# Optimization experiments

Hardware: AMD Instinct MI355X
Metric: run time of the kernel (lower is better)

The kernel has to match this reference:

```python
import jax, jax.numpy as jnp
import numpy as np

H = 16  # num_heads
LN_EPS = 1e-5


def setup_inputs() -> dict:
    key = jax.random.key(0)
    ks = jax.random.split(key, 9)
    B, Lq, Lkv, D = 8, 512, 1024, 1024
    s = 1.0 / np.sqrt(D)
    return {
        "query": jax.random.normal(ks[0], (B, Lq, D), dtype=jnp.float32),
        "key": jax.random.normal(ks[1], (B, Lkv, D), dtype=jnp.float32),
        "value": jax.random.normal(ks[2], (B, Lkv, D), dtype=jnp.float32),
        "in_proj_w": jax.random.normal(ks[3], (3 * D, D), dtype=jnp.float32) * s,
        "in_proj_b": jnp.zeros((3 * D,), dtype=jnp.float32),
        "out_proj_w": jax.random.normal(ks[4], (D, D), dtype=jnp.float32) * s,
        "out_proj_b": jnp.zeros((D,), dtype=jnp.float32),
        "ln_gamma": jnp.ones((D,), dtype=jnp.float32),
        "ln_beta": jnp.zeros((D,), dtype=jnp.float32),
    }


def reference(query, key, value, in_proj_w, in_proj_b, out_proj_w, out_proj_b, ln_gamma, ln_beta):
    B, Lq, D = query.shape
    Lkv = key.shape[1]
    hd = D // H
    wq, wk, wv = jnp.split(in_proj_w, 3, axis=0)   # each [D, D]
    bq, bk, bv = jnp.split(in_proj_b, 3, axis=0)

    def heads(x, L):
        return x.reshape(B, L, H, hd).transpose(0, 2, 1, 3)  # [B,H,L,hd]

    q = heads(query @ wq.T + bq, Lq) * (1.0 / np.sqrt(hd))
    k = heads(key @ wk.T + bk, Lkv)
    v = heads(value @ wv.T + bv, Lkv)

    scores = jnp.einsum('bhqd,bhkd->bhqk', q, k)           # [B,H,Lq,Lkv]
    attn = jax.nn.softmax(scores, axis=-1)
    # attention dropout: identity in eval mode
    ctx = jnp.einsum('bhqk,bhkd->bhqd', attn, v)           # [B,H,Lq,hd]
    ctx = ctx.transpose(0, 2, 1, 3).reshape(B, Lq, D)
    attn_out = ctx @ out_proj_w.T + out_proj_b

    # residual dropout: identity in eval mode; then LayerNorm
    x = query + attn_out
    mu = jnp.mean(x, axis=-1, keepdims=True)
    var = jnp.mean(jnp.square(x - mu), axis=-1, keepdims=True)
    output = (x - mu) * jax.lax.rsqrt(var + LN_EPS) * ln_gamma + ln_beta

    attn_weights = attn.mean(axis=1)                        # avg over heads [B,Lq,Lkv]
    return (output, attn_weights)
```

## Files before the change

kernel.cpp:

```cpp
#include <hip/hip_runtime.h>
#include <stdint.h>

typedef __attribute__((ext_vector_type(8))) short short8;
typedef __attribute__((ext_vector_type(4))) float f32x4;

#define DEV static __device__ __forceinline__

DEV unsigned short f2bf(float f) {
    union { float f; unsigned int u; } v; v.f = f;
    unsigned int u = v.u;
    return (unsigned short)((u + 0x7fffu + ((u >> 16) & 1u)) >> 16);
}

DEV float bf2f(unsigned short s) {
    union { unsigned int u; float f; } v; v.u = ((unsigned int)s) << 16;
    return v.f;
}

DEV void async_lds16(const void* g, void* l) {
    __builtin_amdgcn_global_load_lds(
        (const __attribute__((address_space(1))) unsigned int*)g,
        (__attribute__((address_space(3))) unsigned int*)l, 16, 0, 0);
}

__global__ __launch_bounds__(256)
void k_cvt_all(const float* __restrict__ s0, unsigned short* __restrict__ d0,
               const float* __restrict__ s1, unsigned short* __restrict__ d1,
               const float* __restrict__ s2, unsigned short* __restrict__ d2,
               const float* __restrict__ s3, unsigned short* __restrict__ d3,
               const float* __restrict__ s4, unsigned short* __restrict__ d4)
{
    const float* srcs[5] = {s0, s1, s2, s3, s4};
    unsigned short* dsts[5] = {d0, d1, d2, d3, d4};
    const int n4s[5] = {4096 * 256, 8192 * 256, 8192 * 256, 3072 * 256, 1024 * 256};
    int tid = blockIdx.x * 256 + threadIdx.x;
    int stride = gridDim.x * 256;
#pragma unroll
    for (int seg = 0; seg < 5; ++seg) {
        const float* in = srcs[seg];
        unsigned short* out = dsts[seg];
        int n4 = n4s[seg];
        for (int i = tid; i < n4; i += stride) {
            float4 v = ((const float4*)in)[i];
            ushort4 o;
            o.x = f2bf(v.x); o.y = f2bf(v.y); o.z = f2bf(v.z); o.w = f2bf(v.w);
            ((ushort4*)out)[i] = o;
        }
    }
}

template<typename EpiF>
DEV void gemm_core(const unsigned short* __restrict__ A,
                   const unsigned short* __restrict__ Bm,
                   const float* __restrict__ bias,
                   int row0, int col0,
                   unsigned short* As, unsigned short* Bs,
                   EpiF epi)
{
    const int t = threadIdx.x;
    const int lane = t & 63, w = t >> 6;
    const int i16 = lane & 15, g = lane >> 4;
    const int wr = w >> 1, wc = w & 1;
    const int K = 1024;

    f32x4 acc[4][4];
#pragma unroll
    for (int a = 0; a < 4; ++a)
#pragma unroll
        for (int b = 0; b < 4; ++b) acc[a][b] = f32x4{0.f, 0.f, 0.f, 0.f};

    for (int kt = 0; kt < K / 64; ++kt) {
        const unsigned short* Ag = A + (size_t)row0 * K + kt * 64;
        const unsigned short* Bg = Bm + (size_t)col0 * K + kt * 64;
#pragma unroll
        for (int s = 0; s < 4; ++s) {
            int ch = s * 256 + t;
            int r = ch >> 3, cb = (ch & 7) * 8;
            async_lds16(Ag + (size_t)r * K + cb, &As[ch * 8]);
            async_lds16(Bg + (size_t)r * K + cb, &Bs[ch * 8]);
        }
        __syncthreads();
#pragma unroll
        for (int ks = 0; ks < 2; ++ks) {
            short8 af[4], bfr[4];
#pragma unroll
            for (int mi = 0; mi < 4; ++mi)
                af[mi] = *(const short8*)&As[(wr * 64 + mi * 16 + i16) * 64 + ks * 32 + g * 8];
#pragma unroll
            for (int ni = 0; ni < 4; ++ni)
                bfr[ni] = *(const short8*)&Bs[(wc * 64 + ni * 16 + i16) * 64 + ks * 32 + g * 8];
#pragma unroll
            for (int mi = 0; mi < 4; ++mi)
#pragma unroll
                for (int ni = 0; ni < 4; ++ni)
                    acc[mi][ni] = __builtin_amdgcn_mfma_f32_16x16x32_bf16(af[mi], bfr[ni], acc[mi][ni], 0, 0, 0);
        }
        __syncthreads();
    }

#pragma unroll
    for (int mi = 0; mi < 4; ++mi)
#pragma unroll
        for (int ni = 0; ni < 4; ++ni)
#pragma unroll
            for (int r = 0; r < 4; ++r) {
                int row = row0 + wr * 64 + mi * 16 + g * 4 + r;
                int col = col0 + wc * 64 + ni * 16 + i16;
                epi(row, col, acc[mi][ni][r] + bias[col]);
            }
}

__global__ __launch_bounds__(256)
void k_gemm_qkv(const unsigned short* __restrict__ Aq,
                const unsigned short* __restrict__ Ak,
                const unsigned short* __restrict__ Av,
                const unsigned short* __restrict__ Bm,
                const float* __restrict__ inb,
                unsigned short* __restrict__ q_flat,
                unsigned short* __restrict__ k_heads,
                unsigned short* __restrict__ vt_heads)
{
    __shared__ unsigned short As[128 * 64];
    __shared__ unsigned short Bs[128 * 64];
    const int z = blockIdx.z;
    if (z == 0 && blockIdx.x >= 32) return;
    const int row0 = blockIdx.x * 128;
    const int col0 = blockIdx.y * 128;
    const unsigned short* A = (z == 0) ? Aq : (z == 1) ? Ak : Av;
    const unsigned short* B = Bm + (size_t)z * 1024 * 1024;
    const float* bias = inb + z * 1024;

    if (z == 0) {
        gemm_core(A, B, bias, row0, col0, As, Bs,
            [&](int row, int col, float v) {
                q_flat[(size_t)row * 1024 + col] = f2bf(v * 0.125f);
            });
    } else if (z == 1) {
        gemm_core(A, B, bias, row0, col0, As, Bs,
            [&](int row, int col, float v) {
                int bb = row >> 10, kv = row & 1023, h = col >> 6, d = col & 63;
                size_t addr = (size_t)(bb * 16 + h) * 65536
                            + (size_t)(kv >> 4) * 1024 + (d >> 5) * 512
                            + ((d >> 3) & 3) * 128 + (kv & 15) * 8 + (d & 7);
                k_heads[addr] = f2bf(v);
            });
    } else {
        gemm_core(A, B, bias, row0, col0, As, Bs,
            [&](int row, int col, float v) {
                int bb = row >> 10, kv = row & 1023, h = col >> 6, d = col & 63;
                size_t addr = (size_t)(bb * 16 + h) * 65536
                            + (size_t)(kv >> 5) * 2048 + ((kv >> 3) & 3) * 512
                            + (d >> 4) * 128 + (d & 15) * 8 + (kv & 7);
                vt_heads[addr] = f2bf(v);
            });
    }
}

__global__ __launch_bounds__(256)
void k_gemm_out(const unsigned short* __restrict__ A,
                const unsigned short* __restrict__ Bm,
                const float* __restrict__ bias,
                const float* __restrict__ resid,
                float* __restrict__ Cout)
{
    __shared__ unsigned short As[128 * 64];
    __shared__ unsigned short Bs[128 * 64];
    const int row0 = blockIdx.x * 128;
    const int col0 = blockIdx.y * 128;
    gemm_core(A, Bm, bias, row0, col0, As, Bs,
        [&](int row, int col, float v) {
            Cout[(size_t)row * 1024 + col] = v + resid[(size_t)row * 1024 + col];
        });
}

__global__ __launch_bounds__(512)
void k_attn(const unsigned short* __restrict__ qf,
            const unsigned short* __restrict__ kh,
            const unsigned short* __restrict__ vt,
            unsigned short* __restrict__ ctx,
            unsigned short* __restrict__ attw_part)
{
    __shared__ unsigned short q_lds[16 * 256];
    __shared__ unsigned short p_lds[16 * 1024];
    __shared__ float ctxbuf[16][68];
    __shared__ float redsum[8][16];
    __shared__ float gsum[16];

    const int t = threadIdx.x;
    const int lane = t & 63, w = t >> 6;
    const int i16 = lane & 15, g = lane >> 4;
    const int bid = blockIdx.x;
    const int logical = (bid & 7) * 128 + (bid >> 3);
    const int qt = logical & 31;
    const int bh = logical >> 5;
    const int b = bh >> 2, hg = bh & 3;
    const int q0 = qt * 16;
    const int wn = w & 3, khf = w >> 2;

    {
        const unsigned short* qg = qf + ((size_t)(b * 512 + q0)) * 1024 + hg * 256;
        int q = t >> 5, c = t & 31;
        int sc = (c * 8) ^ ((q & 7) << 3);
        async_lds16(qg + (size_t)q * 1024 + sc, &q_lds[t * 8]);
    }
    __syncthreads();

    float attw_acc[8][4];
#pragma unroll
    for (int mt = 0; mt < 8; ++mt)
#pragma unroll
        for (int r = 0; r < 4; ++r) attw_acc[mt][r] = 0.f;

    for (int hh = 0; hh < 4; ++hh) {
        const int h = hg * 4 + hh;
        short8 qb0, qb1;
        {
            int sw = (i16 & 7) << 4;
            const char* qb = (const char*)q_lds + i16 * 512;
            qb0 = *(const short8*)(qb + ((hh * 128 + g * 16) ^ sw));
            qb1 = *(const short8*)(qb + ((hh * 128 + 64 + g * 16) ^ sw));
        }
        const unsigned short* kbase = kh + (size_t)(b * 16 + h) * 65536
                                    + (size_t)w * 8192 + g * 128 + i16 * 8;
        f32x4 c[8];
#pragma unroll
        for (int mt = 0; mt < 8; ++mt) c[mt] = f32x4{0.f, 0.f, 0.f, 0.f};
#pragma unroll
        for (int mt = 0; mt < 8; ++mt) {
            short8 a0 = *(const short8*)(kbase + mt * 1024);
            short8 a1 = *(const short8*)(kbase + mt * 1024 + 512);
            c[mt] = __builtin_amdgcn_mfma_f32_16x16x32_bf16(a0, qb0, c[mt], 0, 0, 0);
            c[mt] = __builtin_amdgcn_mfma_f32_16x16x32_bf16(a1, qb1, c[mt], 0, 0, 0);
        }
        float s = 0.f;
#pragma unroll
        for (int mt = 0; mt < 8; ++mt)
#pragma unroll
            for (int r = 0; r < 4; ++r) {
                float ev = __expf(c[mt][r]);
                c[mt][r] = ev;
                s += ev;
            }
        s += __shfl_xor(s, 16);
        s += __shfl_xor(s, 32);
        if (lane < 16) redsum[w][lane] = s;
#pragma unroll
        for (int mt = 0; mt < 8; ++mt) {
            unsigned int lo = (unsigned int)f2bf(c[mt][0]) | ((unsigned int)f2bf(c[mt][1]) << 16);
            unsigned int hi = (unsigned int)f2bf(c[mt][2]) | ((unsigned int)f2bf(c[mt][3]) << 16);
            uint2 pk; pk.x = lo; pk.y = hi;
            int pwb = (i16 * 2048 + w * 256 + mt * 32 + g * 8) ^ ((i16 & 7) << 4);
            *(uint2*)((char*)p_lds + pwb) = pk;
        }
        __syncthreads();
        float gs = 0.f;
#pragma unroll
        for (int ww = 0; ww < 8; ++ww) gs += redsum[ww][i16];
        if (w == 0 && lane < 16) gsum[lane] = gs;
        float rs16 = 0.0625f / gs;
#pragma unroll
        for (int mt = 0; mt < 8; ++mt)
#pragma unroll
            for (int r = 0; r < 4; ++r) attw_acc[mt][r] += c[mt][r] * rs16;
        const unsigned short* vbase = vt + (size_t)(b * 16 + h) * 65536
                                    + (size_t)khf * 32768 + g * 512 + wn * 128 + i16 * 8;
        f32x4 cc0 = f32x4{0.f, 0.f, 0.f, 0.f};
        f32x4 cc1 = f32x4{0.f, 0.f, 0.f, 0.f};
#pragma unroll
        for (int kt = 0; kt < 16; kt += 2) {
            short8 pa0 = *(const short8*)((const char*)p_lds
                          + ((i16 * 2048 + khf * 1024 + kt * 64 + g * 16) ^ ((i16 & 7) << 4)));
            short8 vv0 = *(const short8*)(vbase + kt * 2048);
            cc0 = __builtin_amdgcn_mfma_f32_16x16x32_bf16(pa0, vv0, cc0, 0, 0, 0);
            short8 pa1 = *(const short8*)((const char*)p_lds
                          + ((i16 * 2048 + khf * 1024 + (kt + 1) * 64 + g * 16) ^ ((i16 & 7) << 4)));
            short8 vv1 = *(const short8*)(vbase + (kt + 1) * 2048);
            cc1 = __builtin_amdgcn_mfma_f32_16x16x32_bf16(pa1, vv1, cc1, 0, 0, 0);
        }
        if (khf == 0) {
#pragma unroll
            for (int r = 0; r < 4; ++r) ctxbuf[g * 4 + r][wn * 16 + i16] = cc0[r] + cc1[r];
        }
        __syncthreads();
        if (khf == 1) {
#pragma unroll
            for (int r = 0; r < 4; ++r) {
                int q = g * 4 + r;
                float v = cc0[r] + cc1[r] + ctxbuf[q][wn * 16 + i16];
                ctx[((size_t)b * 512 + q0 + q) * 1024 + h * 64 + wn * 16 + i16] = f2bf(v / gsum[q]);
            }
        }
    }

    unsigned short* pw = attw_part + (size_t)hg * (8u * 512u * 1024u)
                       + ((size_t)(b * 512 + q0 + i16)) * 1024;
#pragma unroll
    for (int mt = 0; mt < 8; ++mt) {
        ushort4 o;
        o.x = f2bf(attw_acc[mt][0]); o.y = f2bf(attw_acc[mt][1]);
        o.z = f2bf(attw_acc[mt][2]); o.w = f2bf(attw_acc[mt][3]);
        int kv = w * 128 + mt * 16 + g * 4;
        *(ushort4*)&pw[kv] = o;
    }
}

__global__ __launch_bounds__(256)
void k_attw_red(const unsigned short* __restrict__ part, float* __restrict__ attw) {
    const size_t GSTRIDE = (size_t)8 * 512 * 1024;
    int n4 = (int)(GSTRIDE / 4);
    int i = blockIdx.x * 256 + threadIdx.x;
    int stride = gridDim.x * 256;
    for (; i < n4; i += stride) {
        float4 acc = {0.f, 0.f, 0.f, 0.f};
#pragma unroll
        for (int gp = 0; gp < 4; ++gp) {
            ushort4 u = ((const ushort4*)(part + gp * GSTRIDE))[i];
            acc.x += bf2f(u.x); acc.y += bf2f(u.y);
            acc.z += bf2f(u.z); acc.w += bf2f(u.w);
        }
        ((float4*)attw)[i] = acc;
    }
}

__global__ __launch_bounds__(256)
void k_ln(const float* __restrict__ x, const float* __restrict__ gamma,
          const float* __restrict__ beta, float* __restrict__ out)
{
    int row = blockIdx.x;
    const float* xr = x + (size_t)row * 1024;
    int t = threadIdx.x;
    float4 v = ((const float4*)xr)[t];
    float s = v.x + v.y + v.z + v.w;
    float sq = v.x * v.x + v.y * v.y + v.z * v.z + v.w * v.w;
#pragma unroll
    for (int o = 32; o > 0; o >>= 1) { s += __shfl_xor(s, o); sq += __shfl_xor(sq, o); }
    __shared__ float rs[4], rq[4];
    int w = t >> 6;
    if ((t & 63) == 0) { rs[w] = s; rq[w] = sq; }
    __syncthreads();
    s = rs[0] + rs[1] + rs[2] + rs[3];
    sq = rq[0] + rq[1] + rq[2] + rq[3];
    float mu = s * (1.f / 1024.f);
    float var = sq * (1.f / 1024.f) - mu * mu;
    float rstd = rsqrtf(var + 1e-5f);
    float4 gm = ((const float4*)gamma)[t];
    float4 bt = ((const float4*)beta)[t];
    float4 o;
    o.x = (v.x - mu) * rstd * gm.x + bt.x;
    o.y = (v.y - mu) * rstd * gm.y + bt.y;
    o.z = (v.z - mu) * rstd * gm.z + bt.z;
    o.w = (v.w - mu) * rstd * gm.w + bt.w;
    ((float4*)(out + (size_t)row * 1024))[t] = o;
}

extern "C" void kernel_launch(void* const* d_in, const int* in_sizes, int n_in,
                              void* d_out, int out_size, void* d_ws, size_t ws_size,
                              hipStream_t stream) {
    const float* query = (const float*)d_in[0];
    const float* key   = (const float*)d_in[1];
    const float* value = (const float*)d_in[2];
    const float* inw   = (const float*)d_in[3];
    const float* inb   = (const float*)d_in[4];
    const float* outw  = (const float*)d_in[5];
    const float* outb  = (const float*)d_in[6];
    const float* lng   = (const float*)d_in[7];
    const float* lnb   = (const float*)d_in[8];

    char* ws = (char*)d_ws;
    unsigned short* query_bf = (unsigned short*)(ws);
    unsigned short* key_bf   = (unsigned short*)(ws + ((size_t)8 << 20));
    unsigned short* value_bf = (unsigned short*)(ws + ((size_t)24 << 20));
    unsigned short* inw_bf   = (unsigned short*)(ws + ((size_t)40 << 20));
    unsigned short* outw_bf  = (unsigned short*)(ws + ((size_t)46 << 20));
    unsigned short* q_flat   = (unsigned short*)(ws + ((size_t)48 << 20));
    unsigned short* k_heads  = (unsigned short*)(ws + ((size_t)56 << 20));
    unsigned short* vt_heads = (unsigned short*)(ws + ((size_t)72 << 20));
    unsigned short* ctx_bf   = query_bf;
    unsigned short* attw_part= key_bf;
    float*          x_f32    = (float*)(ws + ((size_t)24 << 20));

    float* out0 = (float*)d_out;
    float* attw = out0 + (size_t)4096 * 1024;

    k_cvt_all<<<dim3(2048), dim3(256), 0, stream>>>(
        query, query_bf, key, key_bf, value, value_bf, inw, inw_bf, outw, outw_bf);

    k_gemm_qkv<<<dim3(64, 8, 3), dim3(256), 0, stream>>>(
        query_bf, key_bf, value_bf, inw_bf, inb, q_flat, k_heads, vt_heads);

    k_attn<<<dim3(1024), dim3(512), 0, stream>>>(q_flat, k_heads, vt_heads, ctx_bf, attw_part);
    k_attw_red<<<dim3(2048), dim3(256), 0, stream>>>(attw_part, attw);

    k_gemm_out<<<dim3(32, 8), dim3(256), 0, stream>>>(ctx_bf, outw_bf, outb, query, x_f32);
    k_ln<<<dim3(4096), dim3(256), 0, stream>>>(x_f32, lng, lnb, out0);
}
```

Baseline: 341.3 us.

## Stage K/V GEMM epilogues through LDS, remap grid, shrink out-proj tiles

The QKV GEMM epilogue for K and V now writes the bf16 results into LDS in the head-blocked layout, then copies them to global memory as contiguous 16-byte stores, replacing scattered 2-byte writes. The grid becomes 1D with a blockIdx remap that drops the idle z==0 blocks and interleaves tiles across XCDs. The output projection moves to 128x64 tiles with 512 blocks to raise occupancy on the small 4096x1024 GEMM. The cost is an extra LDS round trip and barrier in the epilogue.

```diff
diff --git a/kernel.cpp b/kernel.cpp
--- a/kernel.cpp
+++ b/kernel.cpp
@@ -49,13 +49,12 @@
     }
 }
 
-template<typename EpiF>
+template<typename FinF>
 DEV void gemm_core(const unsigned short* __restrict__ A,
                    const unsigned short* __restrict__ Bm,
-                   const float* __restrict__ bias,
                    int row0, int col0,
                    unsigned short* As, unsigned short* Bs,
-                   EpiF epi)
+                   FinF finish)
 {
     const int t = threadIdx.x;
     const int lane = t & 63, w = t >> 6;
@@ -97,17 +96,7 @@
         }
         __syncthreads();
     }
-
-#pragma unroll
-    for (int mi = 0; mi < 4; ++mi)
-#pragma unroll
-        for (int ni = 0; ni < 4; ++ni)
-#pragma unroll
-            for (int r = 0; r < 4; ++r) {
-                int row = row0 + wr * 64 + mi * 16 + g * 4 + r;
-                int col = col0 + wc * 64 + ni * 16 + i16;
-                epi(row, col, acc[mi][ni][r] + bias[col]);
-            }
+    finish(acc);
 }
 
 __global__ __launch_bounds__(256)
@@ -120,38 +109,97 @@
                 unsigned short* __restrict__ k_heads,
                 unsigned short* __restrict__ vt_heads)
 {
-    __shared__ unsigned short As[128 * 64];
-    __shared__ unsigned short Bs[128 * 64];
-    const int z = blockIdx.z;
-    if (z == 0 && blockIdx.x >= 32) return;
-    const int row0 = blockIdx.x * 128;
-    const int col0 = blockIdx.y * 128;
+    __shared__ __align__(16) unsigned short As[128 * 64];
+    __shared__ __align__(16) unsigned short Bs[128 * 64];
+    const int t = threadIdx.x;
+    const int lane = t & 63, w = t >> 6;
+    const int i16 = lane & 15, g = lane >> 4;
+    const int wr = w >> 1, wc = w & 1;
+
+    int l = (blockIdx.x & 7) * 160 + (blockIdx.x >> 3);
+    int z, x, y;
+    if (l < 256)      { z = 0; x = l & 31; y = l >> 5; }
+    else if (l < 768) { z = 1; l -= 256; x = l & 63; y = l >> 6; }
+    else              { z = 2; l -= 768; x = l & 63; y = l >> 6; }
+    const int row0 = x * 128;
+    const int col0 = y * 128;
     const unsigned short* A = (z == 0) ? Aq : (z == 1) ? Ak : Av;
     const unsigned short* B = Bm + (size_t)z * 1024 * 1024;
     const float* bias = inb + z * 1024;
 
     if (z == 0) {
-        gemm_core(A, B, bias, row0, col0, As, Bs,
-            [&](int row, int col, float v) {
-                q_flat[(size_t)row * 1024 + col] = f2bf(v * 0.125f);
+        gemm_core(A, B, row0, col0, As, Bs,
+            [&](const f32x4 (&acc)[4][4]) {
+#pragma unroll
+                for (int mi = 0; mi < 4; ++mi)
+#pragma unroll
+                    for (int ni = 0; ni < 4; ++ni)
+#pragma unroll
+                        for (int r = 0; r < 4; ++r) {
+                            int row = row0 + wr * 64 + mi * 16 + g * 4 + r;
+                            int col = col0 + wc * 64 + ni * 16 + i16;
+                            q_flat[(size_t)row * 1024 + col] = f2bf((acc[mi][ni][r] + bias[col]) * 0.125f);
+                        }
             });
     } else if (z == 1) {
-        gemm_core(A, B, bias, row0, col0, As, Bs,
-            [&](int row, int col, float v) {
-                int bb = row >> 10, kv = row & 1023, h = col >> 6, d = col & 63;
-                size_t addr = (size_t)(bb * 16 + h) * 65536
-                            + (size_t)(kv >> 4) * 1024 + (d >> 5) * 512
-                            + ((d >> 3) & 3) * 128 + (kv & 15) * 8 + (d & 7);
-                k_heads[addr] = f2bf(v);
+        gemm_core(A, B, row0, col0, As, Bs,
+            [&](const f32x4 (&acc)[4][4]) {
+                unsigned short* stg = wc ? Bs : As;
+#pragma unroll
+                for (int mi = 0; mi < 4; ++mi)
+#pragma unroll
+                    for (int ni = 0; ni < 4; ++ni)
+#pragma unroll
+                        for (int r = 0; r < 4; ++r) {
+                            int lkv = wr * 64 + mi * 16 + g * 4 + r;
+                            int d = ni * 16 + i16;
+                            float v = acc[mi][ni][r] + bias[col0 + wc * 64 + d];
+                            int loc = (lkv >> 4) * 1024 + (d >> 5) * 512
+                                    + ((d >> 3) & 3) * 128 + (lkv & 15) * 8 + (d & 7);
+                            stg[loc] = f2bf(v);
+                        }
+                __syncthreads();
+                int bb = row0 >> 10, h0 = col0 >> 6;
+                size_t base = (size_t)(bb * 16 + h0) * 65536 + (size_t)((row0 & 1023) >> 4) * 1024;
+                short8* d0 = (short8*)(k_heads + base);
+                short8* d1 = (short8*)(k_heads + base + 65536);
+#pragma unroll
+                for (int i = 0; i < 4; ++i) {
+                    d0[i * 256 + t] = ((const short8*)As)[i * 256 + t];
+                    d1[i * 256 + t] = ((const short8*)Bs)[i * 256 + t];
+                }
             });
     } else {
-        gemm_core(A, B, bias, row0, col0, As, Bs,
-            [&](int row, int col, float v) {
-                int bb = row >> 10, kv = row & 1023, h = col >> 6, d = col & 63;
-                size_t addr = (size_t)(bb * 16 + h) * 65536
-                            + (size_t)(kv >> 5) * 2048 + ((kv >> 3) & 3) * 512
-                            + (d >> 4) * 128 + (d & 15) * 8 + (kv & 7);
-                vt_heads[addr] = f2bf(v);
+        gemm_core(A, B, row0, col0, As, Bs,
+            [&](const f32x4 (&acc)[4][4]) {
+                unsigned short* stg = wc ? Bs : As;
+#pragma unroll
+                for (int mi = 0; mi < 4; ++mi)
+#pragma unroll
+                    for (int ni = 0; ni < 4; ++ni) {
+                        int lkv0 = wr * 64 + mi * 16 + g * 4;
+                        int d = ni * 16 + i16;
+                        float v0 = acc[mi][ni][0] + bias[col0 + wc * 64 + d];
+                        float v1 = acc[mi][ni][1] + bias[col0 + wc * 64 + d];
+                        float v2 = acc[mi][ni][2] + bias[col0 + wc * 64 + d];
+                        float v3 = acc[mi][ni][3] + bias[col0 + wc * 64 + d];
+                        int loc = (lkv0 >> 5) * 2048 + ((lkv0 >> 3) & 3) * 512
+                                + (d >> 4) * 128 + (d & 15) * 8 + (lkv0 & 7);
+                        uint2 pk;
+                        pk.x = (unsigned int)f2bf(v0) | ((unsigned int)f2bf(v1) << 16);
+                        pk.y = (unsigned int)f2bf(v2) | ((unsigned int)f2bf(v3) << 16);
+                        *(uint2*)&stg[loc] = pk;
+                    }
+                __syncthreads();
+                int bb = row0 >> 10, h0 = col0 >> 6;
+                size_t base = (size_t)(bb * 16 + h0) * 65536 + (size_t)((row0 & 1023) >> 5) * 2048;
+                short8* d0 = (short8*)(vt_heads + base);
+                short8* d1 = (short8*)(vt_heads + base + 65536);
+#pragma unroll
+                for (int i = 0; i < 4; ++i) {
+                    d0[i * 256 + t] = ((const short8*)As)[i * 256 + t];
+                    d1[i * 256 + t] = ((const short8*)Bs)[i * 256 + t];
+                }
             });
     }
 }
@@ -163,14 +211,68 @@
                 const float* __restrict__ resid,
                 float* __restrict__ Cout)
 {
-    __shared__ unsigned short As[128 * 64];
-    __shared__ unsigned short Bs[128 * 64];
-    const int row0 = blockIdx.x * 128;
-    const int col0 = blockIdx.y * 128;
-    gemm_core(A, Bm, bias, row0, col0, As, Bs,
-        [&](int row, int col, float v) {
-            Cout[(size_t)row * 1024 + col] = v + resid[(size_t)row * 1024 + col];
-        });
+    __shared__ __align__(16) unsigned short As[128 * 64];
+    __shared__ __align__(16) unsigned short Bs[64 * 64];
+    const int t = threadIdx.x;
+    const int lane = t & 63, w = t >> 6;
+    const int i16 = lane & 15, g = lane >> 4;
+    const int K = 1024;
+
+    int l = (blockIdx.x & 7) * 64 + (blockIdx.x >> 3);
+    const int row0 = (l & 31) * 128;
+    const int col0 = (l >> 5) * 64;
+
+    f32x4 acc[2][4];
+#pragma unroll
+    for (int a = 0; a < 2; ++a)
+#pragma unroll
+        for (int b = 0; b < 4; ++b) acc[a][b] = f32x4{0.f, 0.f, 0.f, 0.f};
+
+    for (int kt = 0; kt < K / 64; ++kt) {
+        const unsigned short* Ag = A + (size_t)row0 * K + kt * 64;
+        const unsigned short* Bg = Bm + (size_t)col0 * K + kt * 64;
+#pragma unroll
+        for (int s = 0; s < 4; ++s) {
+            int ch = s * 256 + t;
+            int r = ch >> 3, cb = (ch & 7) * 8;
+            async_lds16(Ag + (size_t)r * K + cb, &As[ch * 8]);
+        }
+#pragma unroll
+        for (int s = 0; s < 2; ++s) {
+            int ch = s * 256 + t;
+            int r = ch >> 3, cb = (ch & 7) * 8;
+            async_lds16(Bg + (size_t)r * K + cb, &Bs[ch * 8]);
+        }
+        __syncthreads();
+#pragma unroll
+        for (int ks = 0; ks < 2; ++ks) {
+            short8 af[2], bfr[4];
+#pragma unroll
+            for (int mi = 0; mi < 2; ++mi)
+                af[mi] = *(const short8*)&As[(w * 32 + mi * 16 + i16) * 64 + ks * 32 + g * 8];
+#pragma unroll
+            for (int ni = 0; ni < 4; ++ni)
+                bfr[ni] = *(const short8*)&Bs[(ni * 16 + i16) * 64 + ks * 32 + g * 8];
+#pragma unroll
+            for (int mi = 0; mi < 2; ++mi)
+#pragma unroll
+                for (int ni = 0; ni < 4; ++ni)
+                    acc[mi][ni] = __builtin_amdgcn_mfma_f32_16x16x32_bf16(af[mi], bfr[ni], acc[mi][ni], 0, 0, 0);
+        }
+        __syncthreads();
+    }
+
+#pragma unroll
+    for (int mi = 0; mi < 2; ++mi)
+#pragma unroll
+        for (int ni = 0; ni < 4; ++ni)
+#pragma unroll
+            for (int r = 0; r < 4; ++r) {
+                int row = row0 + w * 32 + mi * 16 + g * 4 + r;
+                int col = col0 + ni * 16 + i16;
+                float v = acc[mi][ni][r] + bias[col];
+                Cout[(size_t)row * 1024 + col] = v + resid[(size_t)row * 1024 + col];
+            }
 }
 
 __global__ __launch_bounds__(512)
@@ -385,12 +487,12 @@
     k_cvt_all<<<dim3(2048), dim3(256), 0, stream>>>(
         query, query_bf, key, key_bf, value, value_bf, inw, inw_bf, outw, outw_bf);
 
-    k_gemm_qkv<<<dim3(64, 8, 3), dim3(256), 0, stream>>>(
+    k_gemm_qkv<<<dim3(1280), dim3(256), 0, stream>>>(
         query_bf, key_bf, value_bf, inw_bf, inb, q_flat, k_heads, vt_heads);
 
     k_attn<<<dim3(1024), dim3(512), 0, stream>>>(q_flat, k_heads, vt_heads, ctx_bf, attw_part);
     k_attw_red<<<dim3(2048), dim3(256), 0, stream>>>(attw_part, attw);
 
-    k_gemm_out<<<dim3(32, 8), dim3(256), 0, stream>>>(ctx_bf, outw_bf, outb, query, x_f32);
+    k_gemm_out<<<dim3(512), dim3(256), 0, stream>>>(ctx_bf, outw_bf, outb, query, x_f32);
     k_ln<<<dim3(4096), dim3(256), 0, stream>>>(x_f32, lng, lnb, out0);
 }
```

Measured after the change: 336.4 us. About the same (-1.4%).
